# Kernel tuning notes

Measured on AMD Instinct MI355X. Metric: run time of the kernel, lower is better.

Reference implementation:

```python
import jax, jax.numpy as jnp
import numpy as np

K = 16
ITERS = 5
DIST_CHUNK = 8  # feature-chunk size to avoid materializing [B,F,S,S]


def pairwise_l1(x):
    """x: [B, F, S] -> d: [B, S, S], d[b,i,j] = ||x[b,:,i]-x[b,:,j]||_1.
    Computed in feature chunks via scan so peak intermediate is [B,CH,S,S]."""
    B, F, S = x.shape
    xc = x.reshape(B, F // DIST_CHUNK, DIST_CHUNK, S).transpose(1, 0, 2, 3)  # [F/CH,B,CH,S]

    def step(acc, blk):  # blk: [B, CH, S]
        return acc + jnp.abs(blk[:, :, :, None] - blk[:, :, None, :]).sum(axis=1), None

    d, _ = jax.lax.scan(step, jnp.zeros((B, S, S), x.dtype), xc)
    return d


def kmedoids_pool(x, w):
    B, F, S = x.shape
    wm = jnp.mean(w, axis=1)                       # [B,S] per-token attention weight
    d = pairwise_l1(x)                             # [B,S,S]
    _, ctr = jax.lax.top_k(wm, K)                  # [B,K] initial medoids
    dw = d * wm[:, None, :]                        # d[b,i,j]*w[b,j]
    for _ in range(ITERS):
        # distance from every token to each current medoid: [B,S,K]
        i2c = jnp.take_along_axis(d, jnp.broadcast_to(ctr[:, None, :], (B, S, K)), axis=2)
        assign = jnp.argmin(i2c, axis=2)           # [B,S] cluster assignment
        member = jax.nn.one_hot(assign, K, dtype=x.dtype)  # [B,S,K]
        # weighted within-cluster cost for candidate i in cluster k:
        # cost[b,i,k] = sum_j d[b,i,j]*w[b,j]*member[b,j,k]
        cost = jnp.einsum('bij,bjk->bik', dw, member)
        cost = jnp.where(member > 0, cost, jnp.inf)  # medoid must be a member
        ctr = jnp.argmin(cost, axis=1)             # [B,K] new medoids
    idx = jnp.broadcast_to(ctr[:, None, :], (B, F, K))
    return jnp.take_along_axis(x, idx, axis=2)     # [B,F,K]


def setup_inputs() -> dict:
    key = jax.random.key(0)
    kx, kw = jax.random.split(key)
    B, F, S = 8, 256, 1024
    x = jax.random.normal(kx, (B, F, S), dtype=jnp.float32)
    w = jax.random.uniform(kw, (B, S, S), dtype=jnp.float32)
    return {"x": x, "w": w}


def reference(x, w):
    return kmedoids_pool(x, w)
```

## Files before the change

### kernel.cpp

```cpp
#include <hip/hip_runtime.h>
#include <math.h>

#define BB 8
#define FF 256
#define SS 1024
#define KK 16
#define ITERS 5

typedef unsigned long long ull;

#define ICH 8
__global__ void wm_part_kernel(const float* __restrict__ w, float* __restrict__ part) {
    int j = blockIdx.x * 256 + threadIdx.x;
    int ic = blockIdx.y, b = blockIdx.z;
    const float* wp = w + (size_t)b * SS * SS + (size_t)ic * (SS / ICH) * SS + j;
    float s = 0.f;
#pragma unroll 16
    for (int i = 0; i < SS / ICH; ++i) s += wp[(size_t)i * SS];
    part[((size_t)ic * BB + b) * SS + j] = s;
}

#define FCD 8
__device__ __forceinline__ void async_copy16(const float* g, const float* s) {
    __builtin_amdgcn_global_load_lds((const __attribute__((address_space(1))) void*)g,
                                     (__attribute__((address_space(3))) void*)s, 16, 0, 0);
}

__global__ __launch_bounds__(128, 4) void dist_kernel(const float* __restrict__ x,
                                                      float* __restrict__ d) {
    __shared__ float smem[2048];
    int tid = threadIdx.x;
    int wave = tid >> 6, lane = tid & 63;
    int b = blockIdx.y;
    int w = blockIdx.x * 2 + wave;
    int it = 0, rem = w;
    while (rem >= 32 - it) { rem -= 32 - it; ++it; }
    int jt = it + rem;
    int i0 = it * 32, j0 = jt * 32;
    const float* xb = x + (size_t)b * FF * SS;
    float* db = d + (size_t)b * SS * SS;
    float* wbase = smem + wave * 1024;
    int ly = lane >> 3, lx = lane & 7;
    int sFl = lane >> 3, sTk = (lane & 7) * 4;

    float acc[4][4] = {};

    auto stage = [&](int c, int h) {
        float* A = wbase + h * 512;
        const float* base = xb + (size_t)c * FCD * SS + (size_t)sFl * SS;
        async_copy16(base + i0 + sTk, A);
        async_copy16(base + j0 + sTk, A + 256);
    };
    auto compute = [&](int h) {
        const float* A = wbase + h * 512;
        const float* B = A + 256;
#pragma unroll
        for (int f = 0; f < FCD; ++f) {
            float4 a = *(const float4*)(A + f * 32 + ly * 4);
            float4 bb = *(const float4*)(B + f * 32 + lx * 4);
            float av[4] = {a.x, a.y, a.z, a.w};
            float bv[4] = {bb.x, bb.y, bb.z, bb.w};
#pragma unroll
            for (int r = 0; r < 4; ++r)
#pragma unroll
                for (int c = 0; c < 4; ++c)
                    acc[r][c] += fabsf(av[r] - bv[c]);
        }
    };

    stage(0, 0);
#pragma unroll 1
    for (int k = 0; k < FF / FCD - 1; ++k) {
        asm volatile("s_waitcnt lgkmcnt(0)" ::: "memory");
        stage(k + 1, (k + 1) & 1);
        asm volatile("s_waitcnt vmcnt(2)" ::: "memory");
        compute(k & 1);
    }
    asm volatile("s_waitcnt vmcnt(0)" ::: "memory");
    compute(1);

#pragma unroll
    for (int r = 0; r < 4; ++r) {
        float4 v = make_float4(acc[r][0], acc[r][1], acc[r][2], acc[r][3]);
        *(float4*)&db[(size_t)(i0 + ly * 4 + r) * SS + j0 + lx * 4] = v;
    }
    if (it != jt) {
#pragma unroll
        for (int c = 0; c < 4; ++c) {
            float4 v = make_float4(acc[0][c], acc[1][c], acc[2][c], acc[3][c]);
            *(float4*)&db[(size_t)(j0 + lx * 4 + c) * SS + i0 + ly * 4] = v;
        }
    }
}

__global__ __launch_bounds__(1024) void topk_assign_kernel(const float* __restrict__ part,
                                                           float* __restrict__ wm,
                                                           const float* __restrict__ d,
                                                           int* __restrict__ assign) {
    int b = blockIdx.x;
    int tid = threadIdx.x;
    int lane = tid & 63, wv = tid >> 6;
    __shared__ ull red[16];
    __shared__ int ctr_s[KK];
    float v = 0.f;
#pragma unroll
    for (int ic = 0; ic < ICH; ++ic) v += part[((size_t)ic * BB + b) * SS + tid];
    v *= (1.0f / SS);
    wm[b * SS + tid] = v;
    ull key = (((ull)__float_as_uint(v)) << 32) | (ull)(0xFFFFFFFFu - (unsigned)tid);
    for (int k = 0; k < KK; ++k) {
        ull kk = key;
#pragma unroll
        for (int off = 32; off; off >>= 1) {
            ull o = __shfl_down(kk, off, 64);
            if (o > kk) kk = o;
        }
        if (lane == 0) red[wv] = kk;
        __syncthreads();
        if (wv == 0) {
            ull k2 = (lane < 16) ? red[lane] : 0ull;
#pragma unroll
            for (int off = 8; off; off >>= 1) {
                ull o = __shfl_down(k2, off, 64);
                if (o > k2) k2 = o;
            }
            if (lane == 0) red[0] = k2;
        }
        __syncthreads();
        ull W = red[0];
        int widx = (int)(0xFFFFFFFFu - (unsigned)(W & 0xFFFFFFFFu));
        if (tid == widx) key = 0;
        if (tid == 0) ctr_s[k] = widx;
        __syncthreads();
    }
    const float* db = d + (size_t)b * SS * SS;
    float bv = INFINITY;
    int bk = 0;
#pragma unroll
    for (int k = 0; k < KK; ++k) {
        float vv = db[(size_t)ctr_s[k] * SS + tid];
        if (vv < bv) { bv = vv; bk = k; }
    }
    assign[b * SS + tid] = bk;
}

#define RPB 16
__global__ __launch_bounds__(256) void cost_kernel(const float* __restrict__ d,
                                                   const float* __restrict__ wm,
                                                   const int* __restrict__ assign,
                                                   float* __restrict__ cost) {
    int b = blockIdx.y;
    int tid = threadIdx.x;
    int lane = tid & 63, wv = tid >> 6;
    __shared__ float wmv[SS];
    __shared__ int asg[SS];
    *(float4*)&wmv[tid * 4] = *(const float4*)&wm[b * SS + tid * 4];
    *(int4*)&asg[tid * 4] = *(const int4*)&assign[b * SS + tid * 4];
    __syncthreads();
    const float* db = d + (size_t)b * SS * SS;
#pragma unroll
    for (int r = 0; r < RPB / 4; ++r) {
        int i = blockIdx.x * RPB + wv * (RPB / 4) + r;
        int my = asg[i];
        const float* drow = db + (size_t)i * SS;
        float s = 0.f;
#pragma unroll
        for (int c = 0; c < SS / 256; ++c) {
            int j = c * 256 + lane * 4;
            float4 dv = *(const float4*)&drow[j];
            float4 wv4 = *(const float4*)&wmv[j];
            int4 a4 = *(const int4*)&asg[j];
            s += (a4.x == my) ? dv.x * wv4.x : 0.f;
            s += (a4.y == my) ? dv.y * wv4.y : 0.f;
            s += (a4.z == my) ? dv.z * wv4.z : 0.f;
            s += (a4.w == my) ? dv.w * wv4.w : 0.f;
        }
#pragma unroll
        for (int off = 32; off; off >>= 1) s += __shfl_down(s, off, 64);
        if (lane == 0) cost[b * SS + i] = s;
    }
}

__global__ __launch_bounds__(1024) void update_assign_kernel(
        const float* __restrict__ d, const float* __restrict__ cost,
        int* __restrict__ assign, const float* __restrict__ x,
        float* __restrict__ out, int last) {
    int b = blockIdx.y;
    int q = blockIdx.x;
    int tid = threadIdx.x;
    int lane = tid & 63, wv = tid >> 6;
    __shared__ float cost_s[SS];
    __shared__ int assign_s[SS];
    __shared__ int ctr_s[KK];
    __shared__ ull pk[4][256];
    cost_s[tid] = cost[b * SS + tid];
    assign_s[tid] = assign[b * SS + tid];
    __syncthreads();
    ull best = ~0ull;
    int k = wv;
    for (int c = 0; c < SS / 64; ++c) {
        int i = c * 64 + lane;
        if (assign_s[i] == k) {
            ull key = (((ull)__float_as_uint(cost_s[i])) << 32) | (unsigned)i;
            if (key < best) best = key;
        }
    }
#pragma unroll
    for (int off = 32; off; off >>= 1) {
        ull o = __shfl_down(best, off, 64);
        if (o < best) best = o;
    }
    if (lane == 0) ctr_s[k] = (best == ~0ull) ? 0 : (int)(best & 0xFFFFFFFFu);
    __syncthreads();
    const float* db = d + (size_t)b * SS * SS;
    if (!last) {
        int tok = q * 256 + (tid & 255);
        int g = tid >> 8;
        ull bk = ~0ull;
#pragma unroll
        for (int kk = 0; kk < 4; ++kk) {
            int k2 = g * 4 + kk;
            float vv = db[(size_t)ctr_s[k2] * SS + tok];
            ull key = (((ull)__float_as_uint(vv)) << 32) | (unsigned)k2;
            if (key < bk) bk = key;
        }
        pk[g][tid & 255] = bk;
        __syncthreads();
        if (tid < 256) {
            ull m = pk[0][tid];
            if (pk[1][tid] < m) m = pk[1][tid];
            if (pk[2][tid] < m) m = pk[2][tid];
            if (pk[3][tid] < m) m = pk[3][tid];
            assign[b * SS + q * 256 + tid] = (int)(m & 0xFFFFFFFFu);
        }
    } else {
        int e = q * 1024 + tid;
        int f = e / KK, k2 = e % KK;
        out[((size_t)b * FF + f) * KK + k2] = x[((size_t)b * FF + f) * SS + ctr_s[k2]];
    }
}

extern "C" void kernel_launch(void* const* d_in, const int* in_sizes, int n_in,
                              void* d_out, int out_size, void* d_ws, size_t ws_size,
                              hipStream_t stream) {
    const float* x = (const float*)d_in[0];
    const float* w = (const float*)d_in[1];
    float* out = (float*)d_out;

    char* ws = (char*)d_ws;
    float* d = (float*)ws;
    size_t off = (size_t)BB * SS * SS * sizeof(float);
    float* wm = (float*)(ws + off);   off += (size_t)BB * SS * sizeof(float);
    int* assign = (int*)(ws + off);   off += (size_t)BB * SS * sizeof(int);
    float* cost = (float*)(ws + off); off += (size_t)BB * SS * sizeof(float);
    float* part = (float*)(ws + off);

    wm_part_kernel<<<dim3(SS / 256, ICH, BB), 256, 0, stream>>>(w, part);
    dist_kernel<<<dim3(264, BB), 128, 0, stream>>>(x, d);
    topk_assign_kernel<<<BB, 1024, 0, stream>>>(part, wm, d, assign);
    for (int itr = 0; itr < ITERS; ++itr) {
        cost_kernel<<<dim3(SS / RPB, BB), 256, 0, stream>>>(d, wm, assign, cost);
        update_assign_kernel<<<dim3(4, BB), 1024, 0, stream>>>(d, cost, assign, x, out,
                                                               itr == ITERS - 1 ? 1 : 0);
    }
}
```

Measured before the change: 232.1 us.

## Fuse column-mean into dist kernel and merge k-medoid iteration into one kernel

The attention-weight column mean now runs in 4 extra blocks per batch appended to the distance kernel, so the separate wm_part kernel goes away. Each iteration becomes a single kernel: every block reduces the previous per-group medoid partials, recomputes the full assignment itself, computes cost for its 16 rows, and writes per-cluster partial minima. This halves the number of launches in the loop and drops the cost and assign buffers, at the price of every block redundantly reading the 16 medoid rows and reducing assignments. A final small gather kernel produces the output.

```diff
diff --git a/kernel.cpp b/kernel.cpp
--- a/kernel.cpp
+++ b/kernel.cpp
@@ -6,19 +6,11 @@
 #define SS 1024
 #define KK 16
 #define ITERS 5
+#define NG 64
 
 typedef unsigned long long ull;
 
-#define ICH 8
-__global__ void wm_part_kernel(const float* __restrict__ w, float* __restrict__ part) {
-    int j = blockIdx.x * 256 + threadIdx.x;
-    int ic = blockIdx.y, b = blockIdx.z;
-    const float* wp = w + (size_t)b * SS * SS + (size_t)ic * (SS / ICH) * SS + j;
-    float s = 0.f;
-#pragma unroll 16
-    for (int i = 0; i < SS / ICH; ++i) s += wp[(size_t)i * SS];
-    part[((size_t)ic * BB + b) * SS + j] = s;
-}
+__device__ __forceinline__ ull umin64(ull a, ull b) { return a < b ? a : b; }
 
 #define FCD 8
 __device__ __forceinline__ void async_copy16(const float* g, const float* s) {
@@ -27,13 +19,33 @@
 }
 
 __global__ __launch_bounds__(128, 4) void dist_kernel(const float* __restrict__ x,
-                                                      float* __restrict__ d) {
+                                                      float* __restrict__ d,
+                                                      const float* __restrict__ wfull,
+                                                      float* __restrict__ wm) {
+    int b = blockIdx.y;
+    if (blockIdx.x >= 264) {
+        int gthr = (blockIdx.x - 264) * 128 + threadIdx.x;
+        const float* wb = wfull + (size_t)b * SS * SS;
+#pragma unroll
+        for (int h = 0; h < 2; ++h) {
+            int j = gthr + h * 512;
+            const float* col = wb + j;
+            float tot = 0.f;
+            for (int ic = 0; ic < 8; ++ic) {
+                float p = 0.f;
+#pragma unroll 16
+                for (int i = 0; i < 128; ++i) p += col[(size_t)(ic * 128 + i) * SS];
+                tot += p;
+            }
+            wm[b * SS + j] = tot * (1.0f / SS);
+        }
+        return;
+    }
     __shared__ float smem[2048];
     int tid = threadIdx.x;
     int wave = tid >> 6, lane = tid & 63;
-    int b = blockIdx.y;
-    int w = blockIdx.x * 2 + wave;
-    int it = 0, rem = w;
+    int tw = blockIdx.x * 2 + wave;
+    int it = 0, rem = tw;
     while (rem >= 32 - it) { rem -= 32 - it; ++it; }
     int jt = it + rem;
     int i0 = it * 32, j0 = jt * 32;
@@ -93,20 +105,14 @@
     }
 }
 
-__global__ __launch_bounds__(1024) void topk_assign_kernel(const float* __restrict__ part,
-                                                           float* __restrict__ wm,
-                                                           const float* __restrict__ d,
-                                                           int* __restrict__ assign) {
+__global__ __launch_bounds__(1024) void topk_kernel(const float* __restrict__ wm,
+                                                    ull* __restrict__ part0) {
     int b = blockIdx.x;
     int tid = threadIdx.x;
     int lane = tid & 63, wv = tid >> 6;
     __shared__ ull red[16];
     __shared__ int ctr_s[KK];
-    float v = 0.f;
-#pragma unroll
-    for (int ic = 0; ic < ICH; ++ic) v += part[((size_t)ic * BB + b) * SS + tid];
-    v *= (1.0f / SS);
-    wm[b * SS + tid] = v;
+    float v = wm[b * SS + tid];
     ull key = (((ull)__float_as_uint(v)) << 32) | (ull)(0xFFFFFFFFu - (unsigned)tid);
     for (int k = 0; k < KK; ++k) {
         ull kk = key;
@@ -133,110 +139,110 @@
         if (tid == 0) ctr_s[k] = widx;
         __syncthreads();
     }
-    const float* db = d + (size_t)b * SS * SS;
-    float bv = INFINITY;
-    int bk = 0;
-#pragma unroll
-    for (int k = 0; k < KK; ++k) {
-        float vv = db[(size_t)ctr_s[k] * SS + tid];
-        if (vv < bv) { bv = vv; bk = k; }
-    }
-    assign[b * SS + tid] = bk;
-}
-
-#define RPB 16
-__global__ __launch_bounds__(256) void cost_kernel(const float* __restrict__ d,
+    int k = tid >> 6, g = tid & 63;
+    part0[((size_t)b * KK + k) * NG + g] =
+        (g == 0) ? (ull)(unsigned)ctr_s[k] : ~0ull;
+}
+
+__global__ __launch_bounds__(256) void iter_kernel(const float* __restrict__ d,
                                                    const float* __restrict__ wm,
-                                                   const int* __restrict__ assign,
-                                                   float* __restrict__ cost) {
-    int b = blockIdx.y;
+                                                   const ull* __restrict__ pprev,
+                                                   ull* __restrict__ pnext) {
+    int b = blockIdx.y, g = blockIdx.x;
     int tid = threadIdx.x;
     int lane = tid & 63, wv = tid >> 6;
     __shared__ float wmv[SS];
     __shared__ int asg[SS];
+    __shared__ int ctr_s[KK];
+    __shared__ ull m16[KK][17];
+    __shared__ ull rowkey[16];
     *(float4*)&wmv[tid * 4] = *(const float4*)&wm[b * SS + tid * 4];
-    *(int4*)&asg[tid * 4] = *(const int4*)&assign[b * SS + tid * 4];
+    {
+        int k = tid >> 4, s = tid & 15;
+        const ull* pp = &pprev[((size_t)b * KK + k) * NG + s * 4];
+        ull m = umin64(umin64(pp[0], pp[1]), umin64(pp[2], pp[3]));
+        m16[k][s] = m;
+    }
+    __syncthreads();
+    if (tid < KK) {
+        ull m = m16[tid][0];
+#pragma unroll
+        for (int s = 1; s < 16; ++s) m = umin64(m, m16[tid][s]);
+        ctr_s[tid] = (m == ~0ull) ? 0 : (int)(m & 0xFFFFFFFFu);
+    }
     __syncthreads();
     const float* db = d + (size_t)b * SS * SS;
 #pragma unroll
-    for (int r = 0; r < RPB / 4; ++r) {
-        int i = blockIdx.x * RPB + wv * (RPB / 4) + r;
+    for (int t = 0; t < 4; ++t) {
+        int j = t * 256 + tid;
+        ull bk = ~0ull;
+#pragma unroll
+        for (int k = 0; k < KK; ++k) {
+            float vv = db[(size_t)ctr_s[k] * SS + j];
+            ull key = (((ull)__float_as_uint(vv)) << 32) | (unsigned)k;
+            if (key < bk) bk = key;
+        }
+        asg[j] = (int)(bk & 0xFFFFFFFFu);
+    }
+    __syncthreads();
+#pragma unroll
+    for (int r = 0; r < 4; ++r) {
+        int i = g * 16 + wv * 4 + r;
         int my = asg[i];
         const float* drow = db + (size_t)i * SS;
         float s = 0.f;
 #pragma unroll
-        for (int c = 0; c < SS / 256; ++c) {
+        for (int c = 0; c < 4; ++c) {
             int j = c * 256 + lane * 4;
             float4 dv = *(const float4*)&drow[j];
-            float4 wv4 = *(const float4*)&wmv[j];
+            float4 w4 = *(const float4*)&wmv[j];
             int4 a4 = *(const int4*)&asg[j];
-            s += (a4.x == my) ? dv.x * wv4.x : 0.f;
-            s += (a4.y == my) ? dv.y * wv4.y : 0.f;
-            s += (a4.z == my) ? dv.z * wv4.z : 0.f;
-            s += (a4.w == my) ? dv.w * wv4.w : 0.f;
+            s += (a4.x == my) ? dv.x * w4.x : 0.f;
+            s += (a4.y == my) ? dv.y * w4.y : 0.f;
+            s += (a4.z == my) ? dv.z * w4.z : 0.f;
+            s += (a4.w == my) ? dv.w * w4.w : 0.f;
         }
 #pragma unroll
         for (int off = 32; off; off >>= 1) s += __shfl_down(s, off, 64);
-        if (lane == 0) cost[b * SS + i] = s;
-    }
-}
-
-__global__ __launch_bounds__(1024) void update_assign_kernel(
-        const float* __restrict__ d, const float* __restrict__ cost,
-        int* __restrict__ assign, const float* __restrict__ x,
-        float* __restrict__ out, int last) {
-    int b = blockIdx.y;
-    int q = blockIdx.x;
-    int tid = threadIdx.x;
-    int lane = tid & 63, wv = tid >> 6;
-    __shared__ float cost_s[SS];
-    __shared__ int assign_s[SS];
+        if (lane == 0)
+            rowkey[wv * 4 + r] = (((ull)__float_as_uint(s)) << 32) | (unsigned)i;
+    }
+    __syncthreads();
+    if (tid < KK) {
+        ull m = ~0ull;
+#pragma unroll
+        for (int r = 0; r < 16; ++r)
+            if (asg[g * 16 + r] == tid) m = umin64(m, rowkey[r]);
+        pnext[((size_t)b * KK + tid) * NG + g] = m;
+    }
+}
+
+__global__ __launch_bounds__(256) void gather_kernel(const float* __restrict__ x,
+                                                     const ull* __restrict__ pfin,
+                                                     float* __restrict__ out) {
+    int b = blockIdx.y, q = blockIdx.x;
+    int tid = threadIdx.x;
+    __shared__ ull m16[KK][17];
     __shared__ int ctr_s[KK];
-    __shared__ ull pk[4][256];
-    cost_s[tid] = cost[b * SS + tid];
-    assign_s[tid] = assign[b * SS + tid];
-    __syncthreads();
-    ull best = ~0ull;
-    int k = wv;
-    for (int c = 0; c < SS / 64; ++c) {
-        int i = c * 64 + lane;
-        if (assign_s[i] == k) {
-            ull key = (((ull)__float_as_uint(cost_s[i])) << 32) | (unsigned)i;
-            if (key < best) best = key;
-        }
-    }
-#pragma unroll
-    for (int off = 32; off; off >>= 1) {
-        ull o = __shfl_down(best, off, 64);
-        if (o < best) best = o;
-    }
-    if (lane == 0) ctr_s[k] = (best == ~0ull) ? 0 : (int)(best & 0xFFFFFFFFu);
-    __syncthreads();
-    const float* db = d + (size_t)b * SS * SS;
-    if (!last) {
-        int tok = q * 256 + (tid & 255);
-        int g = tid >> 8;
-        ull bk = ~0ull;
-#pragma unroll
-        for (int kk = 0; kk < 4; ++kk) {
-            int k2 = g * 4 + kk;
-            float vv = db[(size_t)ctr_s[k2] * SS + tok];
-            ull key = (((ull)__float_as_uint(vv)) << 32) | (unsigned)k2;
-            if (key < bk) bk = key;
-        }
-        pk[g][tid & 255] = bk;
-        __syncthreads();
-        if (tid < 256) {
-            ull m = pk[0][tid];
-            if (pk[1][tid] < m) m = pk[1][tid];
-            if (pk[2][tid] < m) m = pk[2][tid];
-            if (pk[3][tid] < m) m = pk[3][tid];
-            assign[b * SS + q * 256 + tid] = (int)(m & 0xFFFFFFFFu);
-        }
-    } else {
-        int e = q * 1024 + tid;
-        int f = e / KK, k2 = e % KK;
-        out[((size_t)b * FF + f) * KK + k2] = x[((size_t)b * FF + f) * SS + ctr_s[k2]];
+    {
+        int k = tid >> 4, s = tid & 15;
+        const ull* pp = &pfin[((size_t)b * KK + k) * NG + s * 4];
+        ull m = umin64(umin64(pp[0], pp[1]), umin64(pp[2], pp[3]));
+        m16[k][s] = m;
+    }
+    __syncthreads();
+    if (tid < KK) {
+        ull m = m16[tid][0];
+#pragma unroll
+        for (int s = 1; s < 16; ++s) m = umin64(m, m16[tid][s]);
+        ctr_s[tid] = (m == ~0ull) ? 0 : (int)(m & 0xFFFFFFFFu);
+    }
+    __syncthreads();
+#pragma unroll
+    for (int t = 0; t < 4; ++t) {
+        int e = q * 1024 + t * 256 + tid;
+        int f = e >> 4, k = e & 15;
+        out[((size_t)b * FF + f) * KK + k] = x[((size_t)b * FF + f) * SS + ctr_s[k]];
     }
 }
 
@@ -251,16 +257,14 @@
     float* d = (float*)ws;
     size_t off = (size_t)BB * SS * SS * sizeof(float);
     float* wm = (float*)(ws + off);   off += (size_t)BB * SS * sizeof(float);
-    int* assign = (int*)(ws + off);   off += (size_t)BB * SS * sizeof(int);
-    float* cost = (float*)(ws + off); off += (size_t)BB * SS * sizeof(float);
-    float* part = (float*)(ws + off);
-
-    wm_part_kernel<<<dim3(SS / 256, ICH, BB), 256, 0, stream>>>(w, part);
-    dist_kernel<<<dim3(264, BB), 128, 0, stream>>>(x, d);
-    topk_assign_kernel<<<BB, 1024, 0, stream>>>(part, wm, d, assign);
-    for (int itr = 0; itr < ITERS; ++itr) {
-        cost_kernel<<<dim3(SS / RPB, BB), 256, 0, stream>>>(d, wm, assign, cost);
-        update_assign_kernel<<<dim3(4, BB), 1024, 0, stream>>>(d, cost, assign, x, out,
-                                                               itr == ITERS - 1 ? 1 : 0);
-    }
-}
+    off = (off + 15) & ~(size_t)15;
+    ull* part = (ull*)(ws + off);
+    const size_t PST = (size_t)BB * KK * NG;
+
+    dist_kernel<<<dim3(268, BB), 128, 0, stream>>>(x, d, w, wm);
+    topk_kernel<<<BB, 1024, 0, stream>>>(wm, part);
+    for (int t = 1; t <= ITERS; ++t)
+        iter_kernel<<<dim3(NG, BB), 256, 0, stream>>>(d, wm, part + (t - 1) * PST,
+                                                      part + t * PST);
+    gather_kernel<<<dim3(4, BB), 256, 0, stream>>>(x, part + ITERS * PST, out);
+}
```

New measurement: 241.5 us. 4.0% more time.
